# Kernel tuning notes

Measured on AMD Instinct MI355X. Metric: run time of the kernel, lower is better.

## Reference

```python
import jax, jax.numpy as jnp
import numpy as np

B, T, D = 128, 256, 1024   # batch, input_steps, input_dim
H, V, S = 1024, 1024, 128  # hidden_dim, output_dim, output_seq_length


def setup_inputs() -> dict:
    key = jax.random.key(0)
    ks = jax.random.split(key, 16)
    def w(k, shape, fan_in):
        bound = 1.0 / np.sqrt(fan_in)
        return jax.random.uniform(k, shape, jnp.float32, -bound, bound)
    return {
        "h": jax.random.normal(ks[0], (B, T, D), jnp.float32),
        # linear_h_a: Linear(D, H, bias=False); torch weight is (out, in)
        "w_h_a": w(ks[1], (H, D), D),
        # linear_s_a: Linear(H, H, bias=True)
        "w_s_a": w(ks[2], (H, H), H),
        "b_s_a": w(ks[3], (H,), H),
        # linear_a: Linear(H, 1, bias=False)
        "w_a": w(ks[4], (1, H), H),
        # linear_init_s: Linear(D, H, bias=True)
        "w_init_s": w(ks[5], (H, D), D),
        "b_init_s": w(ks[6], (H,), D),
        # GRUCell(V + D, H)
        "gru_w_ih": w(ks[7], (3 * H, V + D), H),
        "gru_w_hh": w(ks[8], (3 * H, H), H),
        "gru_b_ih": w(ks[9], (3 * H,), H),
        "gru_b_hh": w(ks[10], (3 * H,), H),
        # RNNCell(H + D, V), tanh nonlinearity
        "rnn_w_ih": w(ks[11], (V, H + D), V),
        "rnn_w_hh": w(ks[12], (V, V), V),
        "rnn_b_ih": w(ks[13], (V,), V),
        "rnn_b_hh": w(ks[14], (V,), V),
    }


def reference(h, w_h_a, w_s_a, b_s_a, w_a, w_init_s, b_init_s,
              gru_w_ih, gru_w_hh, gru_b_ih, gru_b_hh,
              rnn_w_ih, rnn_w_hh, rnn_b_ih, rnn_b_hh):
    wh = jnp.einsum('btd,hd->bth', h, w_h_a)                 # precomputed W_h @ h
    s0 = jnp.tanh(h[:, 0, :] @ w_init_s.T + b_init_s)        # (B, H)
    y0 = jnp.zeros((h.shape[0], rnn_w_ih.shape[0]), h.dtype)  # (B, V)

    def step(carry, _):
        s, y = carry
        # additive (Bahdanau) attention scores over input steps
        e = jnp.tanh(wh + (s @ w_s_a.T + b_s_a)[:, None, :])  # (B, T, H)
        scores = jnp.einsum('bth,h->bt', e, w_a[0])           # (B, T)
        a = jax.nn.softmax(scores, axis=1)
        c = jnp.einsum('bt,btd->bd', a, h)                    # context (B, D)
        # GRUCell: input = [c, y_prev], hidden = s
        x = jnp.concatenate([c, y], axis=1)
        gi = x @ gru_w_ih.T + gru_b_ih
        gh = s @ gru_w_hh.T + gru_b_hh
        ir, iz, inn = jnp.split(gi, 3, axis=1)
        hr, hz, hn = jnp.split(gh, 3, axis=1)
        r = jax.nn.sigmoid(ir + hr)
        z = jax.nn.sigmoid(iz + hz)
        n = jnp.tanh(inn + r * hn)
        s_new = (1.0 - z) * n + z * s
        # RNNCell(tanh): input = [c, s_new], hidden = y_prev; then softmax
        xr = jnp.concatenate([c, s_new], axis=1)
        pre = xr @ rnn_w_ih.T + rnn_b_ih + y @ rnn_w_hh.T + rnn_b_hh
        y_new = jax.nn.softmax(jnp.tanh(pre), axis=1)
        return (s_new, y_new), y_new

    _, ys = jax.lax.scan(step, (s0, y0), None, length=S)      # ys: (S, B, V)
    return jnp.transpose(ys, (1, 0, 2))                       # (B, S, V)
```

## Files before the change

kernel.cpp:

```cpp
#include <hip/hip_runtime.h>

typedef __bf16 bf16;
typedef __bf16 v8bf __attribute__((ext_vector_type(8)));
typedef __bf16 v4bf __attribute__((ext_vector_type(4)));
typedef float  v4f  __attribute__((ext_vector_type(4)));


static __device__ __forceinline__ float fast_tanh(float x) {
  x = fminf(fmaxf(x, -10.f), 10.f);
  float e = __expf(2.f * x);
  return (e - 1.f) * __builtin_amdgcn_rcpf(e + 1.f);
}
static __device__ __forceinline__ float fast_sigmoid(float x) {
  return __builtin_amdgcn_rcpf(1.f + __expf(-x));
}

static __device__ __forceinline__ size_t packOff(int r, int k) {
  return ((size_t)((r >> 4) * 32 + (k >> 5)) * 64 + ((k >> 3) & 3) * 16 + (r & 15)) * 8 + (k & 7);
}

template<int NKS>
static __device__ __forceinline__ void gemmTile(const bf16* __restrict__ Ap,
                                                const bf16* __restrict__ Bp,
                                                int m0, int n0, int ks0,
                                                v4f acc[2][2]) {
  const int lane = threadIdx.x & 63;
  const int w = threadIdx.x >> 6;
  const int wr = w >> 1, wc = w & 1;
  const bf16* a0p = Ap + (((size_t)((m0 >> 4) + wr * 2) * 32 + ks0) * 64 + lane) * 8;
  const bf16* b0p = Bp + (((size_t)((n0 >> 4) + wc * 2) * 32 + ks0) * 64 + lane) * 8;
#pragma unroll 8
  for (int ks = 0; ks < NKS; ks++) {
    v8bf a0 = *(const v8bf*)(a0p);
    v8bf a1 = *(const v8bf*)(a0p + 16384);
    v8bf b0 = *(const v8bf*)(b0p);
    v8bf b1 = *(const v8bf*)(b0p + 16384);
    a0p += 512; b0p += 512;
    acc[0][0] = __builtin_amdgcn_mfma_f32_16x16x32_bf16(a0, b0, acc[0][0], 0, 0, 0);
    acc[0][1] = __builtin_amdgcn_mfma_f32_16x16x32_bf16(a0, b1, acc[0][1], 0, 0, 0);
    acc[1][0] = __builtin_amdgcn_mfma_f32_16x16x32_bf16(a1, b0, acc[1][0], 0, 0, 0);
    acc[1][1] = __builtin_amdgcn_mfma_f32_16x16x32_bf16(a1, b1, acc[1][1], 0, 0, 0);
  }
}

static __device__ __forceinline__ void storeTileF32(float* __restrict__ C, int ldc,
                                                    int m0, int n0, v4f acc[2][2]) {
  const int lane = threadIdx.x & 63, w = threadIdx.x >> 6;
  const int wr = w >> 1, wc = w & 1;
  const int mB = m0 + wr * 32 + (lane >> 4) * 4;
  const int nB = n0 + wc * 32 + (lane & 15);
#pragma unroll
  for (int mf = 0; mf < 2; mf++)
#pragma unroll
    for (int nf = 0; nf < 2; nf++)
#pragma unroll
      for (int i = 0; i < 4; i++)
        C[(size_t)(mB + mf * 16 + i) * ldc + nB + nf * 16] = acc[mf][nf][i];
}

__global__ __launch_bounds__(256) void kPack(const float* __restrict__ src, int ld,
                                             bf16* __restrict__ dst, int nTh) {
  int th = blockIdx.x * 256 + threadIdx.x;
  if (th >= nTh) return;
  int rb = th >> 11, ks = (th >> 6) & 31, l = th & 63;
  int r = rb * 16 + (l & 15);
  int k = ks * 32 + ((l >> 4) & 3) * 8;
  const float* s = src + (size_t)r * ld + k;
  v4f v0 = *(const v4f*)(s);
  v4f v1 = *(const v4f*)(s + 4);
  v8bf o;
#pragma unroll
  for (int e = 0; e < 4; e++) { o[e] = (bf16)v0[e]; o[4 + e] = (bf16)v1[e]; }
  *(v8bf*)(dst + (size_t)th * 8) = o;
}

__global__ __launch_bounds__(256) void kCast4(const float* __restrict__ src,
                                              bf16* __restrict__ dst, int n4) {
  int i = blockIdx.x * 256 + threadIdx.x;
  if (i < n4) {
    v4f v = ((const v4f*)src)[i];
    ((v4bf*)dst)[i] = __builtin_convertvector(v, v4bf);
  }
}

__global__ __launch_bounds__(256) void kPrep(const float* rnn_b_ih, const float* rnn_b_hh,
                                             float* bsum, bf16* y_b16p) {
  int th = blockIdx.x * 256 + threadIdx.x;
  if (th < 16384) {
    v8bf z = {};
    ((v8bf*)y_b16p)[th] = z;
  } else {
    int j = th - 16384;
    bsum[j] = rnn_b_ih[j] + rnn_b_hh[j];
  }
}

__global__ __launch_bounds__(256) void kGemmTW(const bf16* __restrict__ Ap,
                                               const bf16* __restrict__ Bp,
                                               bf16* __restrict__ C) {
  const int nt = blockIdx.x & 15, mt = blockIdx.x >> 4;
  v4f acc[2][2] = {};
  gemmTile<32>(Ap, Bp, mt * 64, nt * 64, 0, acc);
  const int lane = threadIdx.x & 63, w = threadIdx.x >> 6;
  const int wr = w >> 1, wc = w & 1;
  const int mB = mt * 64 + wr * 32 + (lane >> 4) * 4;
  const int nB = nt * 64 + wc * 32 + (lane & 15);
#pragma unroll
  for (int mf = 0; mf < 2; mf++)
#pragma unroll
    for (int nf = 0; nf < 2; nf++)
#pragma unroll
      for (int i = 0; i < 4; i++)
        C[(size_t)(mB + mf * 16 + i) * 1024 + nB + nf * 16] = (bf16)fast_tanh(acc[mf][nf][i]);
}

__global__ __launch_bounds__(256) void kGemmS0(const bf16* __restrict__ Ap,
                                               const bf16* __restrict__ Bp,
                                               const float* __restrict__ bias,
                                               float* __restrict__ sF, bf16* __restrict__ sB) {
  const int nt = blockIdx.x & 15, mt = blockIdx.x >> 4;
  v4f acc[2][2] = {};
  gemmTile<32>(Ap, Bp, mt * 64, nt * 64, 0, acc);
  const int lane = threadIdx.x & 63, w = threadIdx.x >> 6;
  const int wr = w >> 1, wc = w & 1;
  const int mB = mt * 64 + wr * 32 + (lane >> 4) * 4;
  const int nB = nt * 64 + wc * 32 + (lane & 15);
#pragma unroll
  for (int mf = 0; mf < 2; mf++)
#pragma unroll
    for (int nf = 0; nf < 2; nf++) {
      const int n = nB + nf * 16;
      float bv = bias[n];
#pragma unroll
      for (int i = 0; i < 4; i++) {
        const int m = mB + mf * 16 + i;
        float v = fast_tanh(acc[mf][nf][i] + bv);
        size_t pi = packOff(m, n);
        sF[pi] = v;
        sB[pi] = (bf16)v;
      }
    }
}

__global__ __launch_bounds__(256) void kGemmPS(const bf16* __restrict__ Ap,
                                               const bf16* __restrict__ Bp,
                                               float* __restrict__ PS0, float* __restrict__ PS1) {
  const int t = blockIdx.x;
  const int kh = t & 1, mh = (t >> 1) & 1, nt = t >> 2;
  v4f acc[2][2] = {};
  gemmTile<16>(Ap, Bp, mh * 64, nt * 64, kh * 16, acc);
  storeTileF32(kh ? PS1 : PS0, 5120, mh * 64, nt * 64, acc);
}


static __device__ __forceinline__ void outPhase(
    int b, int step,
    const float* __restrict__ PS0, const float* __restrict__ PS1,
    const float* __restrict__ gcp0, const float* __restrict__ gcp1,
    const float* __restrict__ ygp, const float* __restrict__ bsum,
    float* __restrict__ out, bf16* __restrict__ y_b16p, float* smred) {
  const int tid = threadIdx.x, lane = tid & 63, w = tid >> 6;
  const int v0 = tid * 4;
  const size_t o5 = (size_t)b * 5120 + v0;
  const size_t o4 = (size_t)b * 4096 + 3072 + v0;
  v4f pre = *(const v4f*)(PS0 + o5);
  pre += *(const v4f*)(PS1 + o5);
  pre += *(const v4f*)(gcp0 + o4);
  pre += *(const v4f*)(gcp1 + o4);
  pre += *(const v4f*)(ygp + o4);
  pre += *(const v4f*)(bsum + v0);
  float ee[4];
  float psum = 0.f;
#pragma unroll
  for (int i = 0; i < 4; i++) { ee[i] = __expf(fast_tanh(pre[i])); psum += ee[i]; }
#pragma unroll
  for (int off = 32; off; off >>= 1) psum += __shfl_down(psum, off, 64);
  if (lane == 0) smred[w] = psum;
  __syncthreads();
  const float rden = __builtin_amdgcn_rcpf(smred[0] + smred[1] + smred[2] + smred[3]);
  v4f y4;
#pragma unroll
  for (int i = 0; i < 4; i++) y4[i] = ee[i] * rden;
  *(v4f*)(out + ((size_t)b * 128 + step) * 1024 + v0) = y4;
  *(v4bf*)(y_b16p + packOff(b, v0)) = __builtin_convertvector(y4, v4bf);
}

__global__ __launch_bounds__(256) void kScoresOut(
    const float* __restrict__ PS0, const float* __restrict__ PS1,
    const float* __restrict__ b_s_a, const float* __restrict__ w_a,
    const bf16* __restrict__ twb,
    const float* __restrict__ gcp0, const float* __restrict__ gcp1,
    const float* __restrict__ ygp, const float* __restrict__ bsum,
    float* __restrict__ esh_g, float* __restrict__ out,
    bf16* __restrict__ y_b16p, int step) {
  __shared__ float sm[2052];
  const int tid = threadIdx.x, lane = tid & 63, w = tid >> 6;
  if (blockIdx.x >= 256) {
    if (step == 0) return;
    outPhase(blockIdx.x - 256, step - 1, PS0, PS1, gcp0, gcp1, ygp, bsum,
             out, y_b16p, sm + 2048);
    return;
  }
  const int b = blockIdx.x >> 1, half = blockIdx.x & 1;
  float* ts = sm;
  float* wa = sm + 1024;
#pragma unroll
  for (int jj = 0; jj < 4; jj++) {
    int j = tid + jj * 256;
    float sa = PS0[(size_t)b * 5120 + 1024 + j] + PS1[(size_t)b * 5120 + 1024 + j] + b_s_a[j];
    float t = fast_tanh(sa);
    ts[j] = fminf(fmaxf(t, -0.99999994f), 0.99999994f);
    wa[j] = w_a[j];
  }
  __syncthreads();
  float tj[16], wj[16];
  const int h0 = lane * 16;
#pragma unroll
  for (int j = 0; j < 16; j++) { tj[j] = ts[h0 + j]; wj[j] = wa[h0 + j]; }
  const bf16* twB = twb + ((size_t)b * 256 + half * 128 + w * 32) * 1024 + h0;
  for (int ti = 0; ti < 32; ti++) {
    const bf16* p = twB + (size_t)ti * 1024;
    v8bf t8a = *(const v8bf*)p;
    v8bf t8b = *(const v8bf*)(p + 8);
    float acc = 0.f;
#pragma unroll
    for (int j = 0; j < 8; j++) {
      float tv = (float)t8a[j];
      acc += wj[j] * (tv + tj[j]) * __builtin_amdgcn_rcpf(__builtin_fmaf(tv, tj[j], 1.f));
      float tv2 = (float)t8b[j];
      acc += wj[8 + j] * (tv2 + tj[8 + j]) * __builtin_amdgcn_rcpf(__builtin_fmaf(tv2, tj[8 + j], 1.f));
    }
#pragma unroll
    for (int off = 32; off; off >>= 1) acc += __shfl_down(acc, off, 64);
    if (lane == 0) esh_g[(size_t)b * 256 + half * 128 + w * 32 + ti] = __expf(acc);
  }
}

__global__ __launch_bounds__(256) void kCtxY(
    const float* __restrict__ esh_g, const bf16* __restrict__ hb,
    const bf16* __restrict__ y_b16p, const bf16* __restrict__ W2p,
    bf16* __restrict__ c_b16p, float* __restrict__ ygp) {
  __shared__ float sm[1028];
  const int tid = threadIdx.x, lane = tid & 63, w = tid >> 6;
  if (blockIdx.x < 128) {
    const int b = blockIdx.x;
    float ev = esh_g[(size_t)b * 256 + tid];
    sm[tid] = ev;
    float p = ev;
#pragma unroll
    for (int off = 32; off; off >>= 1) p += __shfl_down(p, off, 64);
    if (lane == 0) sm[1024 + w] = p;
    __syncthreads();
    const float rden = __builtin_amdgcn_rcpf(sm[1024] + sm[1025] + sm[1026] + sm[1027]);
    const int d0 = tid * 4;
    const bf16* hp = hb + (size_t)b * 262144 + d0;
    v4f cacc = {};
#pragma unroll 8
    for (int t = 0; t < 256; t++) {
      v4bf h4 = *(const v4bf*)hp;
      hp += 1024;
      cacc += sm[t] * __builtin_convertvector(h4, v4f);
    }
    cacc *= rden;
    *(v4bf*)(c_b16p + packOff(b, d0)) = __builtin_convertvector(cacc, v4bf);
  } else {
    const int tile = blockIdx.x - 128;
    const int nt = tile & 63, mh = tile >> 6;
    v4f acc[2][2] = {};
    gemmTile<32>(y_b16p, W2p, mh * 64, nt * 64, 0, acc);
    storeTileF32(ygp, 4096, mh * 64, nt * 64, acc);
  }
}

__global__ __launch_bounds__(256) void kCGemm(
    const bf16* __restrict__ c_b16p, const bf16* __restrict__ W3p,
    float* __restrict__ gcp0, float* __restrict__ gcp1) {
  const int kh = blockIdx.x & 1, mh = (blockIdx.x >> 1) & 1, nt = blockIdx.x >> 2;
  v4f acc[2][2] = {};
  gemmTile<16>(c_b16p, W3p, mh * 64, nt * 64, kh * 16, acc);
  storeTileF32(kh ? gcp1 : gcp0, 4096, mh * 64, nt * 64, acc);
}

__global__ __launch_bounds__(256) void kGru(
    const float* __restrict__ gcp0, const float* __restrict__ gcp1,
    const float* __restrict__ ygp,
    const float* __restrict__ PS0, const float* __restrict__ PS1,
    const float* __restrict__ gru_b_ih, const float* __restrict__ gru_b_hh,
    float* __restrict__ s_f32p, bf16* __restrict__ s_b16p) {
  const int th = blockIdx.x * 256 + threadIdx.x;
  const int rb = th >> 11, ks = (th >> 6) & 31, l = th & 63;
  const int r = rb * 16 + (l & 15);
  const int j0 = ks * 32 + ((l >> 4) & 3) * 8;
  const float* g0 = gcp0 + (size_t)r * 4096 + j0;
  const float* g1 = gcp1 + (size_t)r * 4096 + j0;
  const float* yg = ygp + (size_t)r * 4096 + j0;
  const float* p0 = PS0 + (size_t)r * 5120 + j0;
  const float* p1 = PS1 + (size_t)r * 5120 + j0;
  const float* bih = gru_b_ih + j0;
  const float* bhh = gru_b_hh + j0;
  float sv[8], sn[8];
  *(v4f*)sv = *(const v4f*)(s_f32p + (size_t)th * 8);
  *(v4f*)(sv + 4) = *(const v4f*)(s_f32p + (size_t)th * 8 + 4);
#pragma unroll
  for (int e = 0; e < 8; e++) {
    float ir  = g0[e] + g1[e] + yg[e] + bih[e];
    float iz  = g0[1024 + e] + g1[1024 + e] + yg[1024 + e] + bih[1024 + e];
    float in_ = g0[2048 + e] + g1[2048 + e] + yg[2048 + e] + bih[2048 + e];
    float hr = p0[2048 + e] + p1[2048 + e] + bhh[e];
    float hz = p0[3072 + e] + p1[3072 + e] + bhh[1024 + e];
    float hn = p0[4096 + e] + p1[4096 + e] + bhh[2048 + e];
    float rg = fast_sigmoid(ir + hr);
    float zg = fast_sigmoid(iz + hz);
    float ng = fast_tanh(in_ + rg * hn);
    sn[e] = (1.f - zg) * ng + zg * sv[e];
  }
  *(v4f*)(s_f32p + (size_t)th * 8) = *(v4f*)sn;
  *(v4f*)(s_f32p + (size_t)th * 8 + 4) = *(v4f*)(sn + 4);
  v8bf sb;
#pragma unroll
  for (int e = 0; e < 8; e++) sb[e] = (bf16)sn[e];
  *(v8bf*)(s_b16p + (size_t)th * 8) = sb;
}

__global__ __launch_bounds__(256) void kOutFinal(
    const float* __restrict__ PS0, const float* __restrict__ PS1,
    const float* __restrict__ gcp0, const float* __restrict__ gcp1,
    const float* __restrict__ ygp, const float* __restrict__ bsum,
    float* __restrict__ out, bf16* __restrict__ y_b16p) {
  __shared__ float smred[4];
  outPhase(blockIdx.x, 127, PS0, PS1, gcp0, gcp1, ygp, bsum, out, y_b16p, smred);
}

extern "C" void kernel_launch(void* const* d_in, const int* in_sizes, int n_in,
                              void* d_out, int out_size, void* d_ws, size_t ws_size,
                              hipStream_t stream) {
  const float* h        = (const float*)d_in[0];
  const float* w_h_a    = (const float*)d_in[1];
  const float* w_s_a    = (const float*)d_in[2];
  const float* b_s_a    = (const float*)d_in[3];
  const float* w_a      = (const float*)d_in[4];
  const float* w_init_s = (const float*)d_in[5];
  const float* b_init_s = (const float*)d_in[6];
  const float* gru_w_ih = (const float*)d_in[7];
  const float* gru_w_hh = (const float*)d_in[8];
  const float* gru_b_ih = (const float*)d_in[9];
  const float* gru_b_hh = (const float*)d_in[10];
  const float* rnn_w_ih = (const float*)d_in[11];
  const float* rnn_w_hh = (const float*)d_in[12];
  const float* rnn_b_ih = (const float*)d_in[13];
  const float* rnn_b_hh = (const float*)d_in[14];
  (void)in_sizes; (void)n_in; (void)out_size; (void)ws_size;

  char* p = (char*)d_ws;
  auto alloc = [&](size_t bytes) { char* r = p; p += (bytes + 255) & ~(size_t)255; return r; };
  bf16* hbig   = (bf16*)alloc(33554432ull * 2);
  bf16* twb    = (bf16*)alloc(33554432ull * 2);
  bf16* h0p    = (bf16*)alloc(131072ull * 2);
  bf16* wbha_p = (bf16*)alloc(1048576ull * 2);
  bf16* wbini_p= (bf16*)alloc(1048576ull * 2);
  bf16* W2p    = (bf16*)alloc(4194304ull * 2);
  bf16* W3p    = (bf16*)alloc(4194304ull * 2);
  bf16* WP5p   = (bf16*)alloc(5242880ull * 2);
  float* PS0   = (float*)alloc(128ull * 5120 * 4);
  float* PS1   = (float*)alloc(128ull * 5120 * 4);
  float* gcp0  = (float*)alloc(128ull * 4096 * 4);
  float* gcp1  = (float*)alloc(128ull * 4096 * 4);
  float* ygp   = (float*)alloc(128ull * 4096 * 4);
  float* esh_g = (float*)alloc(128ull * 256 * 4);
  float* s_f32p= (float*)alloc(131072ull * 4);
  float* bsum  = (float*)alloc(1024ull * 4);
  bf16* s_b16p = (bf16*)alloc(131072ull * 2);
  bf16* y_b16p = (bf16*)alloc(131072ull * 2);
  bf16* c_b16p = (bf16*)alloc(131072ull * 2);
  float* out = (float*)d_out;

  kPack<<<dim3(16384), 256, 0, stream>>>(h, 1024, hbig, 4194304);
  kPack<<<dim3(64),    256, 0, stream>>>(h, 262144, h0p, 16384);
  kPack<<<dim3(512),   256, 0, stream>>>(w_h_a, 1024, wbha_p, 131072);
  kPack<<<dim3(512),   256, 0, stream>>>(w_init_s, 1024, wbini_p, 131072);
  kPack<<<dim3(1536),  256, 0, stream>>>(gru_w_ih, 2048, W3p, 393216);
  kPack<<<dim3(512),   256, 0, stream>>>(rnn_w_ih, 2048, W3p + 3145728, 131072);
  kPack<<<dim3(1536),  256, 0, stream>>>(gru_w_ih + 1024, 2048, W2p, 393216);
  kPack<<<dim3(512),   256, 0, stream>>>(rnn_w_hh, 1024, W2p + 3145728, 131072);
  kPack<<<dim3(512),   256, 0, stream>>>(rnn_w_ih + 1024, 2048, WP5p, 131072);
  kPack<<<dim3(512),   256, 0, stream>>>(w_s_a, 1024, WP5p + 1048576, 131072);
  kPack<<<dim3(1536),  256, 0, stream>>>(gru_w_hh, 1024, WP5p + 2097152, 393216);
  kPrep<<<dim3(68), 256, 0, stream>>>(rnn_b_ih, rnn_b_hh, bsum, y_b16p);

  kGemmTW<<<dim3(8192), 256, 0, stream>>>(hbig, wbha_p, twb);
  kCast4<<<dim3(32768), 256, 0, stream>>>(h, hbig, 8388608);
  kGemmS0<<<dim3(32), 256, 0, stream>>>(h0p, wbini_p, b_init_s, s_f32p, s_b16p);
  kGemmPS<<<dim3(320), 256, 0, stream>>>(s_b16p, WP5p, PS0, PS1);

  for (int step = 0; step < 128; step++) {
    kScoresOut<<<dim3(384), 256, 0, stream>>>(PS0, PS1, b_s_a, w_a, twb,
                                              gcp0, gcp1, ygp, bsum,
                                              esh_g, out, y_b16p, step);
    kCtxY<<<dim3(256), 256, 0, stream>>>(esh_g, hbig, y_b16p, W2p, c_b16p, ygp);
    kCGemm<<<dim3(256), 256, 0, stream>>>(c_b16p, W3p, gcp0, gcp1);
    kGru<<<dim3(64), 256, 0, stream>>>(gcp0, gcp1, ygp, PS0, PS1,
                                       gru_b_ih, gru_b_hh, s_f32p, s_b16p);
    kGemmPS<<<dim3(320), 256, 0, stream>>>(s_b16p, WP5p, PS0, PS1);
  }
  kOutFinal<<<dim3(128), 256, 0, stream>>>(PS0, PS1, gcp0, gcp1, ygp, bsum, out, y_b16p);
}
```

Measured before the change: 8.711 ms.

## Fuse per-step kernel launches into one persistent kernel with grid barriers

Replaces the 640 per-step kernel launches (5 per decoding step) with a single persistent 320-workgroup kernel that loops over all 128 steps and separates phases with an atomic-counter grid barrier. The output-softmax phase is folded into the scores phase using 64 workgroups handling two batch rows each. This removes launch and inter-kernel gap overhead, but adds spin-wait barriers that depend on all 320 workgroups being co-resident, and drops __restrict__ on the buffers written across phases.

New measurement: 34.33 ms. 3.94x slower.

```diff
diff --git a/kernel.cpp b/kernel.cpp
--- a/kernel.cpp
+++ b/kernel.cpp
@@ -43,7 +43,7 @@
   }
 }
 
-static __device__ __forceinline__ void storeTileF32(float* __restrict__ C, int ldc,
+static __device__ __forceinline__ void storeTileF32(float* C, int ldc,
                                                     int m0, int n0, v4f acc[2][2]) {
   const int lane = threadIdx.x & 63, w = threadIdx.x >> 6;
   const int wr = w >> 1, wc = w & 1;
@@ -84,14 +84,16 @@
 }
 
 __global__ __launch_bounds__(256) void kPrep(const float* rnn_b_ih, const float* rnn_b_hh,
-                                             float* bsum, bf16* y_b16p) {
+                                             float* bsum, bf16* y_b16p, unsigned* bar) {
   int th = blockIdx.x * 256 + threadIdx.x;
   if (th < 16384) {
     v8bf z = {};
     ((v8bf*)y_b16p)[th] = z;
-  } else {
+  } else if (th < 17408) {
     int j = th - 16384;
     bsum[j] = rnn_b_ih[j] + rnn_b_hh[j];
+  } else if (th == 17408) {
+    *bar = 0u;
   }
 }
 
@@ -117,7 +119,7 @@
 __global__ __launch_bounds__(256) void kGemmS0(const bf16* __restrict__ Ap,
                                                const bf16* __restrict__ Bp,
                                                const float* __restrict__ bias,
-                                               float* __restrict__ sF, bf16* __restrict__ sB) {
+                                               float* sF, bf16* sB) {
   const int nt = blockIdx.x & 15, mt = blockIdx.x >> 4;
   v4f acc[2][2] = {};
   gemmTile<32>(Ap, Bp, mt * 64, nt * 64, 0, acc);
@@ -144,7 +146,7 @@
 
 __global__ __launch_bounds__(256) void kGemmPS(const bf16* __restrict__ Ap,
                                                const bf16* __restrict__ Bp,
-                                               float* __restrict__ PS0, float* __restrict__ PS1) {
+                                               float* PS0, float* PS1) {
   const int t = blockIdx.x;
   const int kh = t & 1, mh = (t >> 1) & 1, nt = t >> 2;
   v4f acc[2][2] = {};
@@ -152,13 +154,28 @@
   storeTileF32(kh ? PS1 : PS0, 5120, mh * 64, nt * 64, acc);
 }
 
+static __device__ __forceinline__ void gridBarrier(unsigned* bar, unsigned target) {
+  __syncthreads();
+  if (threadIdx.x == 0) {
+    __threadfence();
+    __hip_atomic_fetch_add(bar, 1u, __ATOMIC_RELAXED, __HIP_MEMORY_SCOPE_AGENT);
+    unsigned tries = 0;
+    while (__hip_atomic_load(bar, __ATOMIC_RELAXED, __HIP_MEMORY_SCOPE_AGENT) < target) {
+      __builtin_amdgcn_s_sleep(2);
+      if (++tries > 100000000u) break;
+    }
+    __threadfence();
+  }
+  __syncthreads();
+  __asm__ volatile("" ::: "memory");
+}
 
 static __device__ __forceinline__ void outPhase(
     int b, int step,
-    const float* __restrict__ PS0, const float* __restrict__ PS1,
-    const float* __restrict__ gcp0, const float* __restrict__ gcp1,
-    const float* __restrict__ ygp, const float* __restrict__ bsum,
-    float* __restrict__ out, bf16* __restrict__ y_b16p, float* smred) {
+    const float* PS0, const float* PS1,
+    const float* gcp0, const float* gcp1,
+    const float* ygp, const float* __restrict__ bsum,
+    float* out, bf16* y_b16p, float* smred) {
   const int tid = threadIdx.x, lane = tid & 63, w = tid >> 6;
   const int v0 = tid * 4;
   const size_t o5 = (size_t)b * 5120 + v0;
@@ -185,150 +202,163 @@
   *(v4bf*)(y_b16p + packOff(b, v0)) = __builtin_convertvector(y4, v4bf);
 }
 
-__global__ __launch_bounds__(256) void kScoresOut(
-    const float* __restrict__ PS0, const float* __restrict__ PS1,
+__global__ __launch_bounds__(256, 2) void kStep(
+    const bf16* __restrict__ twb, const bf16* __restrict__ hb,
     const float* __restrict__ b_s_a, const float* __restrict__ w_a,
-    const bf16* __restrict__ twb,
-    const float* __restrict__ gcp0, const float* __restrict__ gcp1,
-    const float* __restrict__ ygp, const float* __restrict__ bsum,
-    float* __restrict__ esh_g, float* __restrict__ out,
-    bf16* __restrict__ y_b16p, int step) {
+    const float* __restrict__ gru_b_ih, const float* __restrict__ gru_b_hh,
+    const float* __restrict__ bsum,
+    const bf16* __restrict__ W2p, const bf16* __restrict__ W3p,
+    const bf16* __restrict__ WP5p,
+    float* PS0, float* PS1, float* gcp0, float* gcp1, float* ygp,
+    float* esh_g, float* s_f32p,
+    bf16* s_b16p, bf16* y_b16p, bf16* c_b16p,
+    float* out, unsigned* bar)
+{
   __shared__ float sm[2052];
+  const int wg = blockIdx.x;
   const int tid = threadIdx.x, lane = tid & 63, w = tid >> 6;
-  if (blockIdx.x >= 256) {
-    if (step == 0) return;
-    outPhase(blockIdx.x - 256, step - 1, PS0, PS1, gcp0, gcp1, ygp, bsum,
-             out, y_b16p, sm + 2048);
-    return;
-  }
-  const int b = blockIdx.x >> 1, half = blockIdx.x & 1;
-  float* ts = sm;
-  float* wa = sm + 1024;
-#pragma unroll
-  for (int jj = 0; jj < 4; jj++) {
-    int j = tid + jj * 256;
-    float sa = PS0[(size_t)b * 5120 + 1024 + j] + PS1[(size_t)b * 5120 + 1024 + j] + b_s_a[j];
-    float t = fast_tanh(sa);
-    ts[j] = fminf(fmaxf(t, -0.99999994f), 0.99999994f);
-    wa[j] = w_a[j];
-  }
-  __syncthreads();
-  float tj[16], wj[16];
-  const int h0 = lane * 16;
-#pragma unroll
-  for (int j = 0; j < 16; j++) { tj[j] = ts[h0 + j]; wj[j] = wa[h0 + j]; }
-  const bf16* twB = twb + ((size_t)b * 256 + half * 128 + w * 32) * 1024 + h0;
-  for (int ti = 0; ti < 32; ti++) {
-    const bf16* p = twB + (size_t)ti * 1024;
-    v8bf t8a = *(const v8bf*)p;
-    v8bf t8b = *(const v8bf*)(p + 8);
-    float acc = 0.f;
-#pragma unroll
-    for (int j = 0; j < 8; j++) {
-      float tv = (float)t8a[j];
-      acc += wj[j] * (tv + tj[j]) * __builtin_amdgcn_rcpf(__builtin_fmaf(tv, tj[j], 1.f));
-      float tv2 = (float)t8b[j];
-      acc += wj[8 + j] * (tv2 + tj[8 + j]) * __builtin_amdgcn_rcpf(__builtin_fmaf(tv2, tj[8 + j], 1.f));
-    }
-#pragma unroll
-    for (int off = 32; off; off >>= 1) acc += __shfl_down(acc, off, 64);
-    if (lane == 0) esh_g[(size_t)b * 256 + half * 128 + w * 32 + ti] = __expf(acc);
-  }
-}
-
-__global__ __launch_bounds__(256) void kCtxY(
-    const float* __restrict__ esh_g, const bf16* __restrict__ hb,
-    const bf16* __restrict__ y_b16p, const bf16* __restrict__ W2p,
-    bf16* __restrict__ c_b16p, float* __restrict__ ygp) {
-  __shared__ float sm[1028];
-  const int tid = threadIdx.x, lane = tid & 63, w = tid >> 6;
-  if (blockIdx.x < 128) {
-    const int b = blockIdx.x;
-    float ev = esh_g[(size_t)b * 256 + tid];
-    sm[tid] = ev;
-    float p = ev;
-#pragma unroll
-    for (int off = 32; off; off >>= 1) p += __shfl_down(p, off, 64);
-    if (lane == 0) sm[1024 + w] = p;
-    __syncthreads();
-    const float rden = __builtin_amdgcn_rcpf(sm[1024] + sm[1025] + sm[1026] + sm[1027]);
-    const int d0 = tid * 4;
-    const bf16* hp = hb + (size_t)b * 262144 + d0;
-    v4f cacc = {};
+  unsigned gen = 0;
+
+  float wj[16];
+  const bf16* twB0 = nullptr;
+  if (wg < 256) {
+    const int b = wg >> 1, half = wg & 1;
+    const int h0 = lane * 16;
+#pragma unroll
+    for (int j = 0; j < 16; j++) wj[j] = w_a[h0 + j];
+    twB0 = twb + ((size_t)b * 256 + half * 128 + w * 32) * 1024 + h0;
+  }
+
+#pragma unroll 1
+  for (int step = 0; step < 128; step++) {
+    if (wg < 256) {
+      const int b = wg >> 1;
+      float* ts = sm;
+#pragma unroll
+      for (int jj = 0; jj < 4; jj++) {
+        int j = tid + jj * 256;
+        float sa = PS0[(size_t)b * 5120 + 1024 + j] + PS1[(size_t)b * 5120 + 1024 + j] + b_s_a[j];
+        float t = fast_tanh(sa);
+        ts[j] = fminf(fmaxf(t, -0.99999994f), 0.99999994f);
+      }
+      __syncthreads();
+      float tj[16];
+      const int h0 = lane * 16;
+#pragma unroll
+      for (int j = 0; j < 16; j++) tj[j] = ts[h0 + j];
+      for (int ti = 0; ti < 32; ti++) {
+        const bf16* p = twB0 + (size_t)ti * 1024;
+        v8bf t8a = *(const v8bf*)p;
+        v8bf t8b = *(const v8bf*)(p + 8);
+        float acc = 0.f;
+#pragma unroll
+        for (int j = 0; j < 8; j++) {
+          float tv = (float)t8a[j];
+          acc += wj[j] * (tv + tj[j]) * __builtin_amdgcn_rcpf(__builtin_fmaf(tv, tj[j], 1.f));
+          float tv2 = (float)t8b[j];
+          acc += wj[8 + j] * (tv2 + tj[8 + j]) * __builtin_amdgcn_rcpf(__builtin_fmaf(tv2, tj[8 + j], 1.f));
+        }
+#pragma unroll
+        for (int off = 32; off; off >>= 1) acc += __shfl_down(acc, off, 64);
+        if (lane == 0) esh_g[(size_t)(wg >> 1) * 256 + (wg & 1) * 128 + w * 32 + ti] = __expf(acc);
+      }
+      __syncthreads();
+    } else if (step > 0) {
+#pragma unroll 1
+      for (int bb = 0; bb < 2; bb++) {
+        outPhase((wg - 256) * 2 + bb, step - 1, PS0, PS1, gcp0, gcp1, ygp, bsum,
+                 out, y_b16p, sm);
+        __syncthreads();
+      }
+    }
+    gridBarrier(bar, (++gen) * 320u);
+
+    if (wg < 128) {
+      const int b = wg;
+      float ev = esh_g[(size_t)b * 256 + tid];
+      sm[tid] = ev;
+      float p = ev;
+#pragma unroll
+      for (int off = 32; off; off >>= 1) p += __shfl_down(p, off, 64);
+      if (lane == 0) sm[1024 + w] = p;
+      __syncthreads();
+      const float rden = __builtin_amdgcn_rcpf(sm[1024] + sm[1025] + sm[1026] + sm[1027]);
+      const int d0 = tid * 4;
+      const bf16* hp = hb + (size_t)b * 262144 + d0;
+      v4f cacc = {};
 #pragma unroll 8
-    for (int t = 0; t < 256; t++) {
-      v4bf h4 = *(const v4bf*)hp;
-      hp += 1024;
-      cacc += sm[t] * __builtin_convertvector(h4, v4f);
-    }
-    cacc *= rden;
-    *(v4bf*)(c_b16p + packOff(b, d0)) = __builtin_convertvector(cacc, v4bf);
-  } else {
-    const int tile = blockIdx.x - 128;
-    const int nt = tile & 63, mh = tile >> 6;
-    v4f acc[2][2] = {};
-    gemmTile<32>(y_b16p, W2p, mh * 64, nt * 64, 0, acc);
-    storeTileF32(ygp, 4096, mh * 64, nt * 64, acc);
-  }
-}
-
-__global__ __launch_bounds__(256) void kCGemm(
-    const bf16* __restrict__ c_b16p, const bf16* __restrict__ W3p,
-    float* __restrict__ gcp0, float* __restrict__ gcp1) {
-  const int kh = blockIdx.x & 1, mh = (blockIdx.x >> 1) & 1, nt = blockIdx.x >> 2;
-  v4f acc[2][2] = {};
-  gemmTile<16>(c_b16p, W3p, mh * 64, nt * 64, kh * 16, acc);
-  storeTileF32(kh ? gcp1 : gcp0, 4096, mh * 64, nt * 64, acc);
-}
-
-__global__ __launch_bounds__(256) void kGru(
-    const float* __restrict__ gcp0, const float* __restrict__ gcp1,
-    const float* __restrict__ ygp,
-    const float* __restrict__ PS0, const float* __restrict__ PS1,
-    const float* __restrict__ gru_b_ih, const float* __restrict__ gru_b_hh,
-    float* __restrict__ s_f32p, bf16* __restrict__ s_b16p) {
-  const int th = blockIdx.x * 256 + threadIdx.x;
-  const int rb = th >> 11, ks = (th >> 6) & 31, l = th & 63;
-  const int r = rb * 16 + (l & 15);
-  const int j0 = ks * 32 + ((l >> 4) & 3) * 8;
-  const float* g0 = gcp0 + (size_t)r * 4096 + j0;
-  const float* g1 = gcp1 + (size_t)r * 4096 + j0;
-  const float* yg = ygp + (size_t)r * 4096 + j0;
-  const float* p0 = PS0 + (size_t)r * 5120 + j0;
-  const float* p1 = PS1 + (size_t)r * 5120 + j0;
-  const float* bih = gru_b_ih + j0;
-  const float* bhh = gru_b_hh + j0;
-  float sv[8], sn[8];
-  *(v4f*)sv = *(const v4f*)(s_f32p + (size_t)th * 8);
-  *(v4f*)(sv + 4) = *(const v4f*)(s_f32p + (size_t)th * 8 + 4);
-#pragma unroll
-  for (int e = 0; e < 8; e++) {
-    float ir  = g0[e] + g1[e] + yg[e] + bih[e];
-    float iz  = g0[1024 + e] + g1[1024 + e] + yg[1024 + e] + bih[1024 + e];
-    float in_ = g0[2048 + e] + g1[2048 + e] + yg[2048 + e] + bih[2048 + e];
-    float hr = p0[2048 + e] + p1[2048 + e] + bhh[e];
-    float hz = p0[3072 + e] + p1[3072 + e] + bhh[1024 + e];
-    float hn = p0[4096 + e] + p1[4096 + e] + bhh[2048 + e];
-    float rg = fast_sigmoid(ir + hr);
-    float zg = fast_sigmoid(iz + hz);
-    float ng = fast_tanh(in_ + rg * hn);
-    sn[e] = (1.f - zg) * ng + zg * sv[e];
-  }
-  *(v4f*)(s_f32p + (size_t)th * 8) = *(v4f*)sn;
-  *(v4f*)(s_f32p + (size_t)th * 8 + 4) = *(v4f*)(sn + 4);
-  v8bf sb;
-#pragma unroll
-  for (int e = 0; e < 8; e++) sb[e] = (bf16)sn[e];
-  *(v8bf*)(s_b16p + (size_t)th * 8) = sb;
-}
-
-__global__ __launch_bounds__(256) void kOutFinal(
-    const float* __restrict__ PS0, const float* __restrict__ PS1,
-    const float* __restrict__ gcp0, const float* __restrict__ gcp1,
-    const float* __restrict__ ygp, const float* __restrict__ bsum,
-    float* __restrict__ out, bf16* __restrict__ y_b16p) {
-  __shared__ float smred[4];
-  outPhase(blockIdx.x, 127, PS0, PS1, gcp0, gcp1, ygp, bsum, out, y_b16p, smred);
+      for (int t = 0; t < 256; t++) {
+        v4bf h4 = *(const v4bf*)hp;
+        hp += 1024;
+        cacc += sm[t] * __builtin_convertvector(h4, v4f);
+      }
+      cacc *= rden;
+      *(v4bf*)(c_b16p + packOff(b, d0)) = __builtin_convertvector(cacc, v4bf);
+      __syncthreads();
+    } else if (wg < 256) {
+      const int tile = wg - 128;
+      const int nt = tile & 63, mh = tile >> 6;
+      v4f acc[2][2] = {};
+      gemmTile<32>(y_b16p, W2p, mh * 64, nt * 64, 0, acc);
+      storeTileF32(ygp, 4096, mh * 64, nt * 64, acc);
+    }
+    gridBarrier(bar, (++gen) * 320u);
+
+    if (wg < 256) {
+      const int kh = wg & 1, mh = (wg >> 1) & 1, nt = wg >> 2;
+      v4f acc[2][2] = {};
+      gemmTile<16>(c_b16p, W3p, mh * 64, nt * 64, kh * 16, acc);
+      storeTileF32(kh ? gcp1 : gcp0, 4096, mh * 64, nt * 64, acc);
+    }
+    gridBarrier(bar, (++gen) * 320u);
+
+    if (wg < 64) {
+      const int th = wg * 256 + tid;
+      const int rb = th >> 11, ks = (th >> 6) & 31, l = th & 63;
+      const int r = rb * 16 + (l & 15);
+      const int j0 = ks * 32 + ((l >> 4) & 3) * 8;
+      const float* g0 = gcp0 + (size_t)r * 4096 + j0;
+      const float* g1 = gcp1 + (size_t)r * 4096 + j0;
+      const float* yg = ygp + (size_t)r * 4096 + j0;
+      const float* p0 = PS0 + (size_t)r * 5120 + j0;
+      const float* p1 = PS1 + (size_t)r * 5120 + j0;
+      const float* bih = gru_b_ih + j0;
+      const float* bhh = gru_b_hh + j0;
+      float sv[8], sn[8];
+      *(v4f*)sv = *(const v4f*)(s_f32p + (size_t)th * 8);
+      *(v4f*)(sv + 4) = *(const v4f*)(s_f32p + (size_t)th * 8 + 4);
+#pragma unroll
+      for (int e = 0; e < 8; e++) {
+        float ir  = g0[e] + g1[e] + yg[e] + bih[e];
+        float iz  = g0[1024 + e] + g1[1024 + e] + yg[1024 + e] + bih[1024 + e];
+        float in_ = g0[2048 + e] + g1[2048 + e] + yg[2048 + e] + bih[2048 + e];
+        float hr = p0[2048 + e] + p1[2048 + e] + bhh[e];
+        float hz = p0[3072 + e] + p1[3072 + e] + bhh[1024 + e];
+        float hn = p0[4096 + e] + p1[4096 + e] + bhh[2048 + e];
+        float rg = fast_sigmoid(ir + hr);
+        float zg = fast_sigmoid(iz + hz);
+        float ng = fast_tanh(in_ + rg * hn);
+        sn[e] = (1.f - zg) * ng + zg * sv[e];
+      }
+      *(v4f*)(s_f32p + (size_t)th * 8) = *(v4f*)sn;
+      *(v4f*)(s_f32p + (size_t)th * 8 + 4) = *(v4f*)(sn + 4);
+      v8bf sb;
+#pragma unroll
+      for (int e = 0; e < 8; e++) sb[e] = (bf16)sn[e];
+      *(v8bf*)(s_b16p + (size_t)th * 8) = sb;
+    }
+    gridBarrier(bar, (++gen) * 320u);
+
+    {
+      const int kh = wg & 1, mh = (wg >> 1) & 1, nt = wg >> 2;
+      v4f acc[2][2] = {};
+      gemmTile<16>(s_b16p, WP5p, mh * 64, nt * 64, kh * 16, acc);
+      storeTileF32(kh ? PS1 : PS0, 5120, mh * 64, nt * 64, acc);
+    }
+    gridBarrier(bar, (++gen) * 320u);
+  }
+
+  if (wg < 128) outPhase(wg, 127, PS0, PS1, gcp0, gcp1, ygp, bsum, out, y_b16p, sm);
 }
 
 extern "C" void kernel_launch(void* const* d_in, const int* in_sizes, int n_in,
@@ -372,6 +402,7 @@
   bf16* s_b16p = (bf16*)alloc(131072ull * 2);
   bf16* y_b16p = (bf16*)alloc(131072ull * 2);
   bf16* c_b16p = (bf16*)alloc(131072ull * 2);
+  unsigned* bar = (unsigned*)alloc(256);
   float* out = (float*)d_out;
 
   kPack<<<dim3(16384), 256, 0, stream>>>(h, 1024, hbig, 4194304);
@@ -385,22 +416,15 @@
   kPack<<<dim3(512),   256, 0, stream>>>(rnn_w_ih + 1024, 2048, WP5p, 131072);
   kPack<<<dim3(512),   256, 0, stream>>>(w_s_a, 1024, WP5p + 1048576, 131072);
   kPack<<<dim3(1536),  256, 0, stream>>>(gru_w_hh, 1024, WP5p + 2097152, 393216);
-  kPrep<<<dim3(68), 256, 0, stream>>>(rnn_b_ih, rnn_b_hh, bsum, y_b16p);
+  kPrep<<<dim3(69), 256, 0, stream>>>(rnn_b_ih, rnn_b_hh, bsum, y_b16p, bar);
 
   kGemmTW<<<dim3(8192), 256, 0, stream>>>(hbig, wbha_p, twb);
   kCast4<<<dim3(32768), 256, 0, stream>>>(h, hbig, 8388608);
   kGemmS0<<<dim3(32), 256, 0, stream>>>(h0p, wbini_p, b_init_s, s_f32p, s_b16p);
   kGemmPS<<<dim3(320), 256, 0, stream>>>(s_b16p, WP5p, PS0, PS1);
 
-  for (int step = 0; step < 128; step++) {
-    kScoresOut<<<dim3(384), 256, 0, stream>>>(PS0, PS1, b_s_a, w_a, twb,
-                                              gcp0, gcp1, ygp, bsum,
-                                              esh_g, out, y_b16p, step);
-    kCtxY<<<dim3(256), 256, 0, stream>>>(esh_g, hbig, y_b16p, W2p, c_b16p, ygp);
-    kCGemm<<<dim3(256), 256, 0, stream>>>(c_b16p, W3p, gcp0, gcp1);
-    kGru<<<dim3(64), 256, 0, stream>>>(gcp0, gcp1, ygp, PS0, PS1,
-                                       gru_b_ih, gru_b_hh, s_f32p, s_b16p);
-    kGemmPS<<<dim3(320), 256, 0, stream>>>(s_b16p, WP5p, PS0, PS1);
-  }
-  kOutFinal<<<dim3(128), 256, 0, stream>>>(PS0, PS1, gcp0, gcp1, ygp, bsum, out, y_b16p);
-}
+  kStep<<<dim3(320), 256, 0, stream>>>(twb, hbig, b_s_a, w_a, gru_b_ih, gru_b_hh,
+                                       bsum, W2p, W3p, WP5p,
+                                       PS0, PS1, gcp0, gcp1, ygp, esh_g, s_f32p,
+                                       s_b16p, y_b16p, c_b16p, out, bar);
+}
```
